# Kernel tuning notes

Hardware: AMD Instinct MI355X
Metric: run time of the kernel (lower is better)

Reference implementation:

```python
import jax, jax.numpy as jnp
import numpy as np

B, N, K, E, H, V = 128, 256, 4, 300, 150, 32000  # batch, nodes/tree, max children, embed, hidden, vocab
DELTA = 1.0


def setup_inputs() -> dict:
    key = jax.random.key(0)
    ks = jax.random.split(key, 8)
    query = jax.random.randint(ks[0], (B, N), 0, V, dtype=jnp.int32)
    pos = jax.random.randint(ks[1], (B, N), 0, V, dtype=jnp.int32)
    neg = jax.random.randint(ks[2], (B, N), 0, V, dtype=jnp.int32)
    # Complete K-ary tree over N nodes: children of node t are {K*t+1, ..., K*t+K} < N; root = node 0.
    ch = np.full((N, K), -1, dtype=np.int32)
    for t in range(N):
        for j in range(K):
            c = K * t + 1 + j
            if c < N:
                ch[t, j] = c
    children = jnp.asarray(ch)
    emb = jax.random.normal(ks[3], (V, E), dtype=jnp.float32) * 0.02
    W_iou = jax.random.normal(ks[4], (E, 3 * H), dtype=jnp.float32) * 0.05
    U_iou = jax.random.normal(ks[5], (H, 3 * H), dtype=jnp.float32) * 0.05
    b_iou = jnp.zeros((3 * H,), jnp.float32)
    W_f = jax.random.normal(ks[6], (E, H), dtype=jnp.float32) * 0.05
    U_f = jax.random.normal(ks[7], (H, H), dtype=jnp.float32) * 0.05
    b_f = jnp.zeros((H,), jnp.float32)
    return {"query": query, "pos": pos, "neg": neg, "children": children,
            "emb": emb, "W_iou": W_iou, "U_iou": U_iou, "b_iou": b_iou,
            "W_f": W_f, "U_f": U_f, "b_f": b_f}


def _childsum_treelstm(x, children, W_iou, U_iou, b_iou, W_f, U_f, b_f):
    """x: [B, N, E] node embeddings. Returns root (c, h): each [B, H]."""
    Bn, Nn, _ = x.shape
    Hh = U_f.shape[0]
    h0 = jnp.zeros((Bn, Nn, Hh), x.dtype)
    c0 = jnp.zeros((Bn, Nn, Hh), x.dtype)

    def step(carry, t):
        h_all, c_all = carry
        ch = children[t]                        # [K] child indices, -1 = padding
        mask = (ch >= 0)
        idx = jnp.where(mask, ch, 0)
        m = mask.astype(x.dtype)[None, :, None]  # [1, K, 1]
        h_k = h_all[:, idx] * m                 # [B, K, H]
        c_k = c_all[:, idx] * m
        h_sum = h_k.sum(axis=1)                 # child-sum h_tilde [B, H]
        x_t = x[:, t]                           # [B, E]
        iou = x_t @ W_iou + h_sum @ U_iou + b_iou
        i, o, u = jnp.split(iou, 3, axis=-1)
        i = jax.nn.sigmoid(i)
        o = jax.nn.sigmoid(o)
        u = jnp.tanh(u)
        # per-child forget gates: f_jk = sigmoid(W_f x_j + U_f h_k + b_f)
        f = jax.nn.sigmoid((x_t @ W_f + b_f)[:, None, :] + h_k @ U_f)  # [B, K, H]
        c_t = i * u + (f * c_k).sum(axis=1)     # c_k already masked
        h_t = o * jnp.tanh(c_t)
        return (h_all.at[:, t].set(h_t), c_all.at[:, t].set(c_t)), None

    # children have larger indices than parents -> process N-1 .. 0 (root last)
    (h_all, c_all), _ = jax.lax.scan(step, (h0, c0), jnp.arange(Nn - 1, -1, -1))
    return c_all[:, 0], h_all[:, 0]


def _cosine(a, b):
    num = (a * b).sum(-1)
    den = jnp.sqrt((a * a).sum(-1) * (b * b).sum(-1)) + 1e-8
    return num / den


def reference(query, pos, neg, children, emb, W_iou, U_iou, b_iou, W_f, U_f, b_f):
    qc, _ = _childsum_treelstm(emb[query], children, W_iou, U_iou, b_iou, W_f, U_f, b_f)
    pc, _ = _childsum_treelstm(emb[pos], children, W_iou, U_iou, b_iou, W_f, U_f, b_f)
    nc, _ = _childsum_treelstm(emb[neg], children, W_iou, U_iou, b_iou, W_f, U_f, b_f)
    a = _cosine(qc, pc)  # [B]
    b = _cosine(qc, nc)  # [B]
    return jax.nn.relu(DELTA - a + b)
```

## Files before the change

### kernel.cpp

```cpp
#include <hip/hip_runtime.h>
#include <hip/hip_bf16.h>

typedef short short8 __attribute__((ext_vector_type(8)));
typedef float floatx4 __attribute__((ext_vector_type(4)));
typedef unsigned short ushort;

#define Bb 128
#define Nn 256
#define Hh 150
#define HK 160
#define Vv 32000
#define NROW 384
#define PROJC 600
#define NINT 64
#define ZROW (Vv + NROW * NINT)

#define WTN 640

__device__ __forceinline__ float sigf(float x) { return 1.0f / (1.0f + __expf(-x)); }
__device__ __forceinline__ float tanhf_(float x) { return 1.0f - 2.0f / (__expf(2.0f * x) + 1.0f); }
__device__ __forceinline__ float bf2f(ushort s) { union { float f; unsigned u; } v; v.u = ((unsigned)s) << 16; return v.f; }
__device__ __forceinline__ ushort f2bf(float f) { __hip_bfloat16 h = __float2bfloat16(f); return *(ushort*)&h; }

__global__ __launch_bounds__(256) void k_prep(
    const float* __restrict__ W_iou, const float* __restrict__ W_f,
    const float* __restrict__ U_iou, const float* __restrict__ U_f,
    const float* __restrict__ b_iou, const float* __restrict__ b_f,
    short* __restrict__ Wt, short* __restrict__ Uti, short* __restrict__ Utf,
    float* __restrict__ biasw, ushort* __restrict__ h_u, float* __restrict__ c_u)
{
    int idx = blockIdx.x * 256 + threadIdx.x;
    const int nWt = WTN * 320, nUi = 464 * 160, nUf = 160 * 160;
    if (idx < nWt) {
        int n = idx / 320, k = idx % 320;
        float v = 0.f;
        if (k < 300) { if (n < 450) v = W_iou[k * 450 + n]; else if (n < 600) v = W_f[k * 150 + (n - 450)]; }
        Wt[idx] = (short)f2bf(v);
    } else if (idx < nWt + nUi) {
        int i2 = idx - nWt; int n = i2 / 160, k = i2 % 160;
        float v = (k < 150 && n < 450) ? U_iou[k * 450 + n] : 0.f;
        Uti[i2] = (short)f2bf(v);
    } else if (idx < nWt + nUi + nUf) {
        int i2 = idx - nWt - nUi; int n = i2 / 160, k = i2 % 160;
        float v = (k < 150) ? U_f[k * 150 + n] : 0.f;
        Utf[i2] = (short)f2bf(v);
    } else if (idx < nWt + nUi + nUf + WTN) {
        int n = idx - nWt - nUi - nUf;
        biasw[n] = n < 450 ? b_iou[n] : (n < 600 ? b_f[n - 450] : 0.f);
    } else if (idx < nWt + nUi + nUf + WTN + HK) {
        int k = idx - (nWt + nUi + nUf + WTN);
        h_u[(long)ZROW * HK + k] = 0;
        c_u[(long)ZROW * HK + k] = 0.f;
    }
}

__global__ __launch_bounds__(256) void k_vproj(
    const float* __restrict__ emb, const short* __restrict__ Wt,
    const float* __restrict__ biasw, ushort* __restrict__ proj)
{
    __shared__ __align__(16) short As[2][32][328];
    const int tid = threadIdx.x;

    const int bid = blockIdx.x;
    const int xcd = bid & 7, li = bid >> 3;
    const int wgid = (xcd < 4 ? xcd * 63 : 252 + (xcd - 4) * 62) + li;

    const int cg = wgid % 5;
    const int rg = wgid / 5;
    const int rowbase = rg * 320;

    const int w = tid >> 6, lane = tid & 63;
    const int m = lane & 15, kq = (lane >> 4) * 8;
    const int t0 = cg * 8 + w * 2;
    const int col0 = t0 * 16 + m;
    const int col1 = col0 + 16;

    short8 bq0[10], bq1[10];
    #pragma unroll
    for (int ks = 0; ks < 10; ks++) {
        bq0[ks] = *(const short8*)(Wt + (long)col0 * 320 + kq + ks * 32);
        bq1[ks] = *(const short8*)(Wt + (long)col1 * 320 + kq + ks * 32);
    }
    const float bias0 = biasw[col0];
    const float bias1 = biasw[col1];

    for (int i = tid; i < 2 * 32 * 5; i += 256) {
        int bz = i / 160, r2 = (i % 160) / 5, kk = (i % 5) * 4;
        *(short4*)&As[bz][r2][300 + kk] = make_short4(0, 0, 0, 0);
    }

    {
        const float4* src = (const float4*)emb + (long)rowbase * 75;
        for (int i = tid; i < 2400; i += 256) {
            int r = i / 75, k0 = (i % 75) * 4;
            float4 x = src[i];
            short4 sv;
            sv.x = (short)f2bf(x.x); sv.y = (short)f2bf(x.y);
            sv.z = (short)f2bf(x.z); sv.w = (short)f2bf(x.w);
            *(short4*)&As[0][r][k0] = sv;
        }
    }
    __syncthreads();

    for (int c = 0; c < 10; c++) {
        const int buf = c & 1;

        float4 x[10];
        if (c < 9) {
            const float4* src = (const float4*)emb + (long)(rowbase + (c + 1) * 32) * 75;
            #pragma unroll
            for (int j = 0; j < 10; j++) {
                int i = tid + j * 256;
                if (i < 2400) x[j] = src[i];
            }
        }

        floatx4 a00 = {0.f,0.f,0.f,0.f}, a01 = a00, a10 = a00, a11 = a00;
        #pragma unroll
        for (int ks = 0; ks < 10; ks++) {
            short8 a0 = *(const short8*)&As[buf][m][kq + ks * 32];
            short8 a1 = *(const short8*)&As[buf][16 + m][kq + ks * 32];
            a00 = __builtin_amdgcn_mfma_f32_16x16x32_bf16(a0, bq0[ks], a00, 0, 0, 0);
            a01 = __builtin_amdgcn_mfma_f32_16x16x32_bf16(a0, bq1[ks], a01, 0, 0, 0);
            a10 = __builtin_amdgcn_mfma_f32_16x16x32_bf16(a1, bq0[ks], a10, 0, 0, 0);
            a11 = __builtin_amdgcn_mfma_f32_16x16x32_bf16(a1, bq1[ks], a11, 0, 0, 0);
        }

        {
            int v0 = rowbase + c * 32;
            int rb = (lane >> 4) * 4;
            if (col0 < PROJC) {
                #pragma unroll
                for (int reg = 0; reg < 4; reg++) {
                    proj[(long)(v0 + rb + reg) * PROJC + col0]      = f2bf(a00[reg] + bias0);
                    proj[(long)(v0 + 16 + rb + reg) * PROJC + col0] = f2bf(a10[reg] + bias0);
                }
            }
            if (col1 < PROJC) {
                #pragma unroll
                for (int reg = 0; reg < 4; reg++) {
                    proj[(long)(v0 + rb + reg) * PROJC + col1]      = f2bf(a01[reg] + bias1);
                    proj[(long)(v0 + 16 + rb + reg) * PROJC + col1] = f2bf(a11[reg] + bias1);
                }
            }
        }

        if (c < 9) {
            #pragma unroll
            for (int j = 0; j < 10; j++) {
                int i = tid + j * 256;
                if (i < 2400) {
                    int r = i / 75, k0 = (i % 75) * 4;
                    short4 sv;
                    sv.x = (short)f2bf(x[j].x); sv.y = (short)f2bf(x[j].y);
                    sv.z = (short)f2bf(x[j].z); sv.w = (short)f2bf(x[j].w);
                    *(short4*)&As[buf ^ 1][r][k0] = sv;
                }
            }
        }
        __syncthreads();
    }
}

__global__ __launch_bounds__(256) void k_vleaf(
    const ushort* __restrict__ proj, ushort* __restrict__ h_u, float* __restrict__ c_u)
{
    int idx = blockIdx.x * 256 + threadIdx.x;
    int v = idx / 20, k0 = (idx % 20) * 8;
    const ushort* pr = proj + (long)v * PROJC;
    ushort hv[8]; float cvv[8];
    #pragma unroll
    for (int e = 0; e < 8; e++) {
        int k = k0 + e;
        if (k < Hh) {
            float iv = sigf(bf2f(pr[k]));
            float ov = sigf(bf2f(pr[150 + k]));
            float uv = tanhf_(bf2f(pr[300 + k]));
            float cc = iv * uv;
            cvv[e] = cc;
            hv[e] = f2bf(ov * tanhf_(cc));
        } else { cvv[e] = 0.f; hv[e] = 0; }
    }
    *(int4*)(h_u + (long)v * HK + k0) = *(int4*)hv;
    *(float4*)(c_u + (long)v * HK + k0)     = make_float4(cvv[0], cvv[1], cvv[2], cvv[3]);
    *(float4*)(c_u + (long)v * HK + k0 + 4) = make_float4(cvv[4], cvv[5], cvv[6], cvv[7]);
}

__global__ __launch_bounds__(256) void k_level(
    int t0,
    const int* __restrict__ tq, const int* __restrict__ tp, const int* __restrict__ tn,
    const int* __restrict__ children, const ushort* __restrict__ proj,
    const short* __restrict__ Uti, const short* __restrict__ Utf,
    ushort* __restrict__ h_u, float* __restrict__ c_u)
{
    __shared__ __align__(16) short As[5][16][168];
    __shared__ int idx_s[16][4];
    __shared__ int tok_s[16];

    const int tid = threadIdx.x;
    const int t = t0 + blockIdx.x / 24;
    const int r0 = (blockIdx.x % 24) * 16;

    if (tid < 64) {
        int r = tid >> 2, j = tid & 3;
        int rg = r0 + r, g = rg >> 7, b = rg & 127;
        const int* tok = (g == 0) ? tq : (g == 1 ? tp : tn);
        int ch = children[t * 4 + j];
        int idx;
        if (ch < 0)        idx = ZROW;
        else if (ch >= 64) idx = tok[b * Nn + ch];
        else               idx = Vv + rg * NINT + ch;
        idx_s[r][j] = idx;
        if (j == 0) tok_s[r] = tok[b * Nn + t];
    }
    __syncthreads();

    for (int i = tid; i < 16 * 20; i += 256) {
        int r = i / 20, k0 = (i % 20) * 8;
        int4 v0 = *(const int4*)(h_u + (long)idx_s[r][0] * HK + k0);
        int4 v1 = *(const int4*)(h_u + (long)idx_s[r][1] * HK + k0);
        int4 v2 = *(const int4*)(h_u + (long)idx_s[r][2] * HK + k0);
        int4 v3 = *(const int4*)(h_u + (long)idx_s[r][3] * HK + k0);
        *(int4*)&As[1][r][k0] = v0;
        *(int4*)&As[2][r][k0] = v1;
        *(int4*)&As[3][r][k0] = v2;
        *(int4*)&As[4][r][k0] = v3;
        ushort s[8];
        const ushort* p0 = (const ushort*)&v0; const ushort* p1 = (const ushort*)&v1;
        const ushort* p2 = (const ushort*)&v2; const ushort* p3 = (const ushort*)&v3;
        #pragma unroll
        for (int e = 0; e < 8; e++)
            s[e] = f2bf(bf2f(p0[e]) + bf2f(p1[e]) + bf2f(p2[e]) + bf2f(p3[e]));
        *(int4*)&As[0][r][k0] = *(int4*)s;
    }
    __syncthreads();

    const int w = tid >> 6, lane = tid & 63;
    const int m = lane & 15, kq = (lane >> 4) * 8;

    for (int nt = w; nt < 10; nt += 4) {
        int col = nt * 16 + m;
        const short* bi  = Uti + (long)(col) * HK + kq;
        const short* bo  = Uti + (long)(150 + col) * HK + kq;
        const short* bu  = Uti + (long)(300 + col) * HK + kq;
        const short* bff = Utf + (long)col * HK + kq;
        floatx4 ai = {0.f,0.f,0.f,0.f}, ao = ai, au = ai;
        floatx4 af0 = ai, af1 = ai, af2 = ai, af3 = ai;
        #pragma unroll
        for (int ks = 0; ks < 5; ks++) {
            short8 asum = *(const short8*)&As[0][m][kq + ks * 32];
            short8 ac0  = *(const short8*)&As[1][m][kq + ks * 32];
            short8 ac1  = *(const short8*)&As[2][m][kq + ks * 32];
            short8 ac2  = *(const short8*)&As[3][m][kq + ks * 32];
            short8 ac3  = *(const short8*)&As[4][m][kq + ks * 32];
            short8 vbi = *(const short8*)(bi + ks * 32);
            short8 vbo = *(const short8*)(bo + ks * 32);
            short8 vbu = *(const short8*)(bu + ks * 32);
            short8 vbf = *(const short8*)(bff + ks * 32);
            ai  = __builtin_amdgcn_mfma_f32_16x16x32_bf16(asum, vbi, ai, 0, 0, 0);
            ao  = __builtin_amdgcn_mfma_f32_16x16x32_bf16(asum, vbo, ao, 0, 0, 0);
            au  = __builtin_amdgcn_mfma_f32_16x16x32_bf16(asum, vbu, au, 0, 0, 0);
            af0 = __builtin_amdgcn_mfma_f32_16x16x32_bf16(ac0,  vbf, af0, 0, 0, 0);
            af1 = __builtin_amdgcn_mfma_f32_16x16x32_bf16(ac1,  vbf, af1, 0, 0, 0);
            af2 = __builtin_amdgcn_mfma_f32_16x16x32_bf16(ac2,  vbf, af2, 0, 0, 0);
            af3 = __builtin_amdgcn_mfma_f32_16x16x32_bf16(ac3,  vbf, af3, 0, 0, 0);
        }

        int rbase = (lane >> 4) * 4;
        if (col < Hh) {
            #pragma unroll
            for (int reg = 0; reg < 4; reg++) {
                int r = rbase + reg, rg = r0 + r;
                const ushort* pr = proj + (long)tok_s[r] * PROJC;
                float iv = sigf(bf2f(pr[col])        + ai[reg]);
                float ov = sigf(bf2f(pr[150 + col])  + ao[reg]);
                float uv = tanhf_(bf2f(pr[300 + col]) + au[reg]);
                float fpre = bf2f(pr[450 + col]);
                float cv = iv * uv;
                cv = fmaf(sigf(fpre + af0[reg]), c_u[(long)idx_s[r][0] * HK + col], cv);
                cv = fmaf(sigf(fpre + af1[reg]), c_u[(long)idx_s[r][1] * HK + col], cv);
                cv = fmaf(sigf(fpre + af2[reg]), c_u[(long)idx_s[r][2] * HK + col], cv);
                cv = fmaf(sigf(fpre + af3[reg]), c_u[(long)idx_s[r][3] * HK + col], cv);
                long o = (long)(Vv + rg * NINT + t) * HK + col;
                c_u[o] = cv;
                h_u[o] = f2bf(ov * tanhf_(cv));
            }
        } else {
            #pragma unroll
            for (int reg = 0; reg < 4; reg++) {
                long o = (long)(Vv + (r0 + rbase + reg) * NINT + t) * HK + col;
                c_u[o] = 0.f; h_u[o] = 0;
            }
        }
    }
}

__global__ __launch_bounds__(64) void k_cos(const float* __restrict__ c_u, float* __restrict__ out)
{
    int b = blockIdx.x, tid = threadIdx.x;
    const float* qc = c_u + (long)(Vv + (0 * Bb + b) * NINT) * HK;
    const float* pc = c_u + (long)(Vv + (1 * Bb + b) * NINT) * HK;
    const float* nc = c_u + (long)(Vv + (2 * Bb + b) * NINT) * HK;
    float qp = 0, qn = 0, qq = 0, pp = 0, nn2 = 0;
    for (int k = tid; k < Hh; k += 64) {
        float qv = qc[k], pv = pc[k], nv = nc[k];
        qp += qv * pv; qn += qv * nv; qq += qv * qv; pp += pv * pv; nn2 += nv * nv;
    }
    #pragma unroll
    for (int off = 32; off > 0; off >>= 1) {
        qp += __shfl_down(qp, off, 64);
        qn += __shfl_down(qn, off, 64);
        qq += __shfl_down(qq, off, 64);
        pp += __shfl_down(pp, off, 64);
        nn2 += __shfl_down(nn2, off, 64);
    }
    if (tid == 0) {
        float a = qp / (sqrtf(qq * pp) + 1e-8f);
        float d = qn / (sqrtf(qq * nn2) + 1e-8f);
        out[b] = fmaxf(0.0f, 1.0f - a + d);
    }
}

extern "C" void kernel_launch(void* const* d_in, const int* in_sizes, int n_in,
                              void* d_out, int out_size, void* d_ws, size_t ws_size,
                              hipStream_t stream)
{
    const int*   tq       = (const int*)d_in[0];
    const int*   tp       = (const int*)d_in[1];
    const int*   tn       = (const int*)d_in[2];
    const int*   children = (const int*)d_in[3];
    const float* emb      = (const float*)d_in[4];
    const float* W_iou    = (const float*)d_in[5];
    const float* U_iou    = (const float*)d_in[6];
    const float* b_iou    = (const float*)d_in[7];
    const float* W_f      = (const float*)d_in[8];
    const float* U_f      = (const float*)d_in[9];
    const float* b_f      = (const float*)d_in[10];
    float* out = (float*)d_out;

    char* ws = (char*)d_ws;
    ushort* proj  = (ushort*)ws;
    ushort* h_u   = (ushort*)(ws + 38400000);
    float*  c_u   = (float*)(ws + 56504640);
    short*  Wt    = (short*)(ws + 92713920);
    short*  Uti   = (short*)(ws + 93123520);
    short*  Utf   = (short*)(ws + 93272000);
    float*  biasw = (float*)(ws + 93323200);

    k_prep<<<1194, 256, 0, stream>>>(W_iou, W_f, U_iou, U_f, b_iou, b_f,
                                     Wt, Uti, Utf, biasw, h_u, c_u);
    k_vproj<<<500, 256, 0, stream>>>(emb, Wt, biasw, proj);
    k_vleaf<<<2500, 256, 0, stream>>>(proj, h_u, c_u);
    k_level<<<43 * 24, 256, 0, stream>>>(21, tq, tp, tn, children, proj, Uti, Utf, h_u, c_u);
    k_level<<<16 * 24, 256, 0, stream>>>(5,  tq, tp, tn, children, proj, Uti, Utf, h_u, c_u);
    k_level<<<4 * 24, 256, 0, stream>>>(1,   tq, tp, tn, children, proj, Uti, Utf, h_u, c_u);
    k_level<<<1 * 24, 256, 0, stream>>>(0,   tq, tp, tn, children, proj, Uti, Utf, h_u, c_u);
    k_cos<<<Bb, 64, 0, stream>>>(c_u, out);
}
```

Measured before the change: 252.2 us.

## Process two tree nodes per level block, reusing U weights held in registers

Each k_level block now handles two nodes of the same level instead of one. The U_iou/U_f B-fragments are loaded into registers once per column tile and reused for both nodes, and the proj and child-c gathers are issued before the MFMA loop so their latency can overlap. This halves the grid size for each level and doubles the shared memory per block. That reduces parallelism on the small upper levels and may lower occupancy through higher LDS and register use.

```diff
diff --git a/kernel.cpp b/kernel.cpp
--- a/kernel.cpp
+++ b/kernel.cpp
@@ -187,22 +187,26 @@
 }
 
 __global__ __launch_bounds__(256) void k_level(
-    int t0,
+    int t_base, int t_cnt,
     const int* __restrict__ tq, const int* __restrict__ tp, const int* __restrict__ tn,
     const int* __restrict__ children, const ushort* __restrict__ proj,
     const short* __restrict__ Uti, const short* __restrict__ Utf,
     ushort* __restrict__ h_u, float* __restrict__ c_u)
 {
-    __shared__ __align__(16) short As[5][16][168];
-    __shared__ int idx_s[16][4];
-    __shared__ int tok_s[16];
+    __shared__ __align__(16) short As[2][5][16][168];
+    __shared__ int idx_s[2][16][4];
+    __shared__ int tok_s[2][16];
 
     const int tid = threadIdx.x;
-    const int t = t0 + blockIdx.x / 24;
+    const int chunk = blockIdx.x / 24;
     const int r0 = (blockIdx.x % 24) * 16;
-
-    if (tid < 64) {
-        int r = tid >> 2, j = tid & 3;
+    const int tA = t_base + chunk * 2;
+    const int nT = min(2, t_base + t_cnt - tA);
+
+    if (tid < 64 * nT) {
+        int tt = tid >> 6, q = tid & 63;
+        int r = q >> 2, j = q & 3;
+        int t = tA + tt;
         int rg = r0 + r, g = rg >> 7, b = rg & 127;
         const int* tok = (g == 0) ? tq : (g == 1 ? tp : tn);
         int ch = children[t * 4 + j];
@@ -210,86 +214,109 @@
         if (ch < 0)        idx = ZROW;
         else if (ch >= 64) idx = tok[b * Nn + ch];
         else               idx = Vv + rg * NINT + ch;
-        idx_s[r][j] = idx;
-        if (j == 0) tok_s[r] = tok[b * Nn + t];
+        idx_s[tt][r][j] = idx;
+        if (j == 0) tok_s[tt][r] = tok[b * Nn + t];
     }
     __syncthreads();
 
-    for (int i = tid; i < 16 * 20; i += 256) {
-        int r = i / 20, k0 = (i % 20) * 8;
-        int4 v0 = *(const int4*)(h_u + (long)idx_s[r][0] * HK + k0);
-        int4 v1 = *(const int4*)(h_u + (long)idx_s[r][1] * HK + k0);
-        int4 v2 = *(const int4*)(h_u + (long)idx_s[r][2] * HK + k0);
-        int4 v3 = *(const int4*)(h_u + (long)idx_s[r][3] * HK + k0);
-        *(int4*)&As[1][r][k0] = v0;
-        *(int4*)&As[2][r][k0] = v1;
-        *(int4*)&As[3][r][k0] = v2;
-        *(int4*)&As[4][r][k0] = v3;
+    for (int i = tid; i < 320 * nT; i += 256) {
+        int tt = i / 320, i2 = i % 320;
+        int r = i2 / 20, k0 = (i2 % 20) * 8;
+        int4 v0 = *(const int4*)(h_u + (long)idx_s[tt][r][0] * HK + k0);
+        int4 v1 = *(const int4*)(h_u + (long)idx_s[tt][r][1] * HK + k0);
+        int4 v2 = *(const int4*)(h_u + (long)idx_s[tt][r][2] * HK + k0);
+        int4 v3 = *(const int4*)(h_u + (long)idx_s[tt][r][3] * HK + k0);
+        *(int4*)&As[tt][1][r][k0] = v0;
+        *(int4*)&As[tt][2][r][k0] = v1;
+        *(int4*)&As[tt][3][r][k0] = v2;
+        *(int4*)&As[tt][4][r][k0] = v3;
         ushort s[8];
         const ushort* p0 = (const ushort*)&v0; const ushort* p1 = (const ushort*)&v1;
         const ushort* p2 = (const ushort*)&v2; const ushort* p3 = (const ushort*)&v3;
         #pragma unroll
         for (int e = 0; e < 8; e++)
             s[e] = f2bf(bf2f(p0[e]) + bf2f(p1[e]) + bf2f(p2[e]) + bf2f(p3[e]));
-        *(int4*)&As[0][r][k0] = *(int4*)s;
+        *(int4*)&As[tt][0][r][k0] = *(int4*)s;
     }
     __syncthreads();
 
     const int w = tid >> 6, lane = tid & 63;
     const int m = lane & 15, kq = (lane >> 4) * 8;
+    const int rbase = (lane >> 4) * 4;
 
     for (int nt = w; nt < 10; nt += 4) {
         int col = nt * 16 + m;
-        const short* bi  = Uti + (long)(col) * HK + kq;
-        const short* bo  = Uti + (long)(150 + col) * HK + kq;
-        const short* bu  = Uti + (long)(300 + col) * HK + kq;
-        const short* bff = Utf + (long)col * HK + kq;
-        floatx4 ai = {0.f,0.f,0.f,0.f}, ao = ai, au = ai;
-        floatx4 af0 = ai, af1 = ai, af2 = ai, af3 = ai;
+
+        short8 Bi[5], Bo[5], Bu[5], Bf[5];
         #pragma unroll
         for (int ks = 0; ks < 5; ks++) {
-            short8 asum = *(const short8*)&As[0][m][kq + ks * 32];
-            short8 ac0  = *(const short8*)&As[1][m][kq + ks * 32];
-            short8 ac1  = *(const short8*)&As[2][m][kq + ks * 32];
-            short8 ac2  = *(const short8*)&As[3][m][kq + ks * 32];
-            short8 ac3  = *(const short8*)&As[4][m][kq + ks * 32];
-            short8 vbi = *(const short8*)(bi + ks * 32);
-            short8 vbo = *(const short8*)(bo + ks * 32);
-            short8 vbu = *(const short8*)(bu + ks * 32);
-            short8 vbf = *(const short8*)(bff + ks * 32);
-            ai  = __builtin_amdgcn_mfma_f32_16x16x32_bf16(asum, vbi, ai, 0, 0, 0);
-            ao  = __builtin_amdgcn_mfma_f32_16x16x32_bf16(asum, vbo, ao, 0, 0, 0);
-            au  = __builtin_amdgcn_mfma_f32_16x16x32_bf16(asum, vbu, au, 0, 0, 0);
-            af0 = __builtin_amdgcn_mfma_f32_16x16x32_bf16(ac0,  vbf, af0, 0, 0, 0);
-            af1 = __builtin_amdgcn_mfma_f32_16x16x32_bf16(ac1,  vbf, af1, 0, 0, 0);
-            af2 = __builtin_amdgcn_mfma_f32_16x16x32_bf16(ac2,  vbf, af2, 0, 0, 0);
-            af3 = __builtin_amdgcn_mfma_f32_16x16x32_bf16(ac3,  vbf, af3, 0, 0, 0);
-        }
-
-        int rbase = (lane >> 4) * 4;
-        if (col < Hh) {
+            Bi[ks] = *(const short8*)(Uti + (long)(col)       * HK + kq + ks * 32);
+            Bo[ks] = *(const short8*)(Uti + (long)(150 + col) * HK + kq + ks * 32);
+            Bu[ks] = *(const short8*)(Uti + (long)(300 + col) * HK + kq + ks * 32);
+            Bf[ks] = *(const short8*)(Utf + (long)(col)       * HK + kq + ks * 32);
+        }
+
+        for (int tt = 0; tt < nT; ++tt) {
+            int t = tA + tt;
+
+            float pv0[4], pv1[4], pv2[4], pv3[4];
+            float cu0[4], cu1[4], cu2[4], cu3[4];
+            if (col < Hh) {
+                #pragma unroll
+                for (int reg = 0; reg < 4; reg++) {
+                    const ushort* pr = proj + (long)tok_s[tt][rbase + reg] * PROJC;
+                    pv0[reg] = bf2f(pr[col]);
+                    pv1[reg] = bf2f(pr[150 + col]);
+                    pv2[reg] = bf2f(pr[300 + col]);
+                    pv3[reg] = bf2f(pr[450 + col]);
+                    cu0[reg] = c_u[(long)idx_s[tt][rbase + reg][0] * HK + col];
+                    cu1[reg] = c_u[(long)idx_s[tt][rbase + reg][1] * HK + col];
+                    cu2[reg] = c_u[(long)idx_s[tt][rbase + reg][2] * HK + col];
+                    cu3[reg] = c_u[(long)idx_s[tt][rbase + reg][3] * HK + col];
+                }
+            }
+
+            floatx4 ai = {0.f,0.f,0.f,0.f}, ao = ai, au = ai;
+            floatx4 af0 = ai, af1 = ai, af2 = ai, af3 = ai;
             #pragma unroll
-            for (int reg = 0; reg < 4; reg++) {
-                int r = rbase + reg, rg = r0 + r;
-                const ushort* pr = proj + (long)tok_s[r] * PROJC;
-                float iv = sigf(bf2f(pr[col])        + ai[reg]);
-                float ov = sigf(bf2f(pr[150 + col])  + ao[reg]);
-                float uv = tanhf_(bf2f(pr[300 + col]) + au[reg]);
-                float fpre = bf2f(pr[450 + col]);
-                float cv = iv * uv;
-                cv = fmaf(sigf(fpre + af0[reg]), c_u[(long)idx_s[r][0] * HK + col], cv);
-                cv = fmaf(sigf(fpre + af1[reg]), c_u[(long)idx_s[r][1] * HK + col], cv);
-                cv = fmaf(sigf(fpre + af2[reg]), c_u[(long)idx_s[r][2] * HK + col], cv);
-                cv = fmaf(sigf(fpre + af3[reg]), c_u[(long)idx_s[r][3] * HK + col], cv);
-                long o = (long)(Vv + rg * NINT + t) * HK + col;
-                c_u[o] = cv;
-                h_u[o] = f2bf(ov * tanhf_(cv));
-            }
-        } else {
-            #pragma unroll
-            for (int reg = 0; reg < 4; reg++) {
-                long o = (long)(Vv + (r0 + rbase + reg) * NINT + t) * HK + col;
-                c_u[o] = 0.f; h_u[o] = 0;
+            for (int ks = 0; ks < 5; ks++) {
+                short8 asum = *(const short8*)&As[tt][0][m][kq + ks * 32];
+                short8 ac0  = *(const short8*)&As[tt][1][m][kq + ks * 32];
+                short8 ac1  = *(const short8*)&As[tt][2][m][kq + ks * 32];
+                short8 ac2  = *(const short8*)&As[tt][3][m][kq + ks * 32];
+                short8 ac3  = *(const short8*)&As[tt][4][m][kq + ks * 32];
+                ai  = __builtin_amdgcn_mfma_f32_16x16x32_bf16(asum, Bi[ks], ai, 0, 0, 0);
+                ao  = __builtin_amdgcn_mfma_f32_16x16x32_bf16(asum, Bo[ks], ao, 0, 0, 0);
+                au  = __builtin_amdgcn_mfma_f32_16x16x32_bf16(asum, Bu[ks], au, 0, 0, 0);
+                af0 = __builtin_amdgcn_mfma_f32_16x16x32_bf16(ac0,  Bf[ks], af0, 0, 0, 0);
+                af1 = __builtin_amdgcn_mfma_f32_16x16x32_bf16(ac1,  Bf[ks], af1, 0, 0, 0);
+                af2 = __builtin_amdgcn_mfma_f32_16x16x32_bf16(ac2,  Bf[ks], af2, 0, 0, 0);
+                af3 = __builtin_amdgcn_mfma_f32_16x16x32_bf16(ac3,  Bf[ks], af3, 0, 0, 0);
+            }
+
+            if (col < Hh) {
+                #pragma unroll
+                for (int reg = 0; reg < 4; reg++) {
+                    int rg = r0 + rbase + reg;
+                    float iv = sigf(pv0[reg] + ai[reg]);
+                    float ov = sigf(pv1[reg] + ao[reg]);
+                    float uv = tanhf_(pv2[reg] + au[reg]);
+                    float fpre = pv3[reg];
+                    float cv = iv * uv;
+                    cv = fmaf(sigf(fpre + af0[reg]), cu0[reg], cv);
+                    cv = fmaf(sigf(fpre + af1[reg]), cu1[reg], cv);
+                    cv = fmaf(sigf(fpre + af2[reg]), cu2[reg], cv);
+                    cv = fmaf(sigf(fpre + af3[reg]), cu3[reg], cv);
+                    long o = (long)(Vv + rg * NINT + t) * HK + col;
+                    c_u[o] = cv;
+                    h_u[o] = f2bf(ov * tanhf_(cv));
+                }
+            } else {
+                #pragma unroll
+                for (int reg = 0; reg < 4; reg++) {
+                    long o = (long)(Vv + (r0 + rbase + reg) * NINT + t) * HK + col;
+                    c_u[o] = 0.f; h_u[o] = 0;
+                }
             }
         }
     }
@@ -351,9 +378,9 @@
                                      Wt, Uti, Utf, biasw, h_u, c_u);
     k_vproj<<<500, 256, 0, stream>>>(emb, Wt, biasw, proj);
     k_vleaf<<<2500, 256, 0, stream>>>(proj, h_u, c_u);
-    k_level<<<43 * 24, 256, 0, stream>>>(21, tq, tp, tn, children, proj, Uti, Utf, h_u, c_u);
-    k_level<<<16 * 24, 256, 0, stream>>>(5,  tq, tp, tn, children, proj, Uti, Utf, h_u, c_u);
-    k_level<<<4 * 24, 256, 0, stream>>>(1,   tq, tp, tn, children, proj, Uti, Utf, h_u, c_u);
-    k_level<<<1 * 24, 256, 0, stream>>>(0,   tq, tp, tn, children, proj, Uti, Utf, h_u, c_u);
+    k_level<<<22 * 24, 256, 0, stream>>>(21, 43, tq, tp, tn, children, proj, Uti, Utf, h_u, c_u);
+    k_level<<<8 * 24, 256, 0, stream>>>(5, 16, tq, tp, tn, children, proj, Uti, Utf, h_u, c_u);
+    k_level<<<2 * 24, 256, 0, stream>>>(1, 4,  tq, tp, tn, children, proj, Uti, Utf, h_u, c_u);
+    k_level<<<1 * 24, 256, 0, stream>>>(0, 1,  tq, tp, tn, children, proj, Uti, Utf, h_u, c_u);
     k_cos<<<Bb, 64, 0, stream>>>(c_u, out);
 }
```

Result: no change. 250.2 us (-0.8%).
